# Kernel tuning notes

Hardware: AMD Instinct MI355X
Metric: run time of the kernel (lower is better)

## Reference

```python
import jax, jax.numpy as jnp
import numpy as np

B, M, D = 2048, 128, 5          # batch, max_atoms, max_degree
F_A, F_B, C = 62, 6, 128        # atom feats, bond feats, conv_width


def setup_inputs() -> dict:
    key = jax.random.key(0)
    k1, k2, k3, k4, k5 = jax.random.split(key, 5)
    atoms = jax.random.normal(k1, (B, M, F_A), dtype=jnp.float32)
    bonds = jax.random.uniform(k2, (B, M, D, F_B), dtype=jnp.float32)
    # edges in [-1, M-1]; -1 = no neighbour (padding)
    edges = jax.random.randint(k3, (B, M, D), 0, M + 1, dtype=jnp.int32) - 1
    fan = F_A + F_B
    scale = float(np.sqrt(2.0 / (fan + C)))
    W_inner = jax.random.normal(k4, (D, fan, C), dtype=jnp.float32) * scale
    b_inner = jnp.zeros((D, C), dtype=jnp.float32)
    W_self = jax.random.normal(k5, (fan, C), dtype=jnp.float32) * scale
    b_self = jnp.zeros((C,), dtype=jnp.float32)
    return {"atoms": atoms, "bonds": bonds, "edges": edges,
            "W_inner": W_inner, "b_inner": b_inner,
            "W_self": W_self, "b_self": b_self}


def reference(atoms, bonds, edges, W_inner, b_inner, W_self, b_self):
    # --- encode() of TiedGraphAutoencoder (encode_only=True) ---
    b = atoms.shape[0]
    # atom degree = number of non-(-1) entries per atom  (B, M)
    deg = jnp.sum((edges != -1).astype(jnp.float32), axis=-1)

    # neighbour_lookup: pad a zero atom at index 0, shift edges by +1,
    # batched gather -> (B, M, D, F_A)
    padded = jnp.pad(atoms, ((0, 0), (1, 0), (0, 0)))
    neigh = padded[jnp.arange(b)[:, None, None], edges + 1]

    summed_atoms = neigh.sum(axis=-2)          # (B, M, F_A)
    summed_bonds = bonds.sum(axis=-2)          # (B, M, F_B)
    summed_features = jnp.concatenate([summed_atoms, summed_bonds], axis=-1)

    # per-degree TimeDistributed Dense + relu, masked by (deg == d), summed
    h = jax.nn.relu(jnp.einsum('bmf,dfc->bmdc', summed_features, W_inner)
                    + b_inner)                 # (B, M, D, C)
    mask = (deg[..., None] == jnp.arange(D, dtype=jnp.float32)).astype(h.dtype)
    zni = jnp.einsum('bmdc,bmd->bmc', h, mask)  # (B, M, C)

    # self connection: dense on [atoms, summed_bonds]
    vxi = jnp.concatenate([atoms, summed_bonds], axis=-1)
    zxi = jax.nn.relu(vxi @ W_self + b_self)    # (B, M, C)

    return zni + zxi
```

## Files before the change

kernel.cpp:

```cpp
#include <hip/hip_runtime.h>

#define NB 2048
#define NM 128
#define ND 5
#define NFA 62
#define NFB 6
#define NFAN 68
#define NC 128
#define KTOT 96

typedef __bf16 bf16x8 __attribute__((ext_vector_type(8)));
typedef float floatx4 __attribute__((ext_vector_type(4)));

__device__ __forceinline__ unsigned short f2bf(float x) {
    unsigned u = __builtin_bit_cast(unsigned, x);
    u += 0x7FFFu + ((u >> 16) & 1u);
    return (unsigned short)(u >> 16);
}

__global__ __launch_bounds__(256) void prep_w(const float* __restrict__ W_self,
                                              unsigned short* __restrict__ wsb) {
    const int i = blockIdx.x * 256 + threadIdx.x;
    const int e     = i & 7;
    const int chunk = i >> 3;
    const int lane  = chunk & 63;
    const int cs    = chunk >> 6;
    const int ct    = cs / 3;
    const int slice = cs - 3 * ct;
    const int quad  = lane >> 4;
    const int col   = lane & 15;
    const int k     = slice * 32 + quad * 8 + e;
    const int c     = ct * 16 + col;
    unsigned short v = 0;
    if (k < NFAN) v = f2bf(W_self[k * NC + c]);
    wsb[i] = v;
}

__device__ __forceinline__ void glds16(const void* g, void* l) {
    __builtin_amdgcn_global_load_lds(
        (const __attribute__((address_space(1))) unsigned int*)g,
        (__attribute__((address_space(3))) unsigned int*)l,
        16, 0, 0);
}

__device__ __forceinline__ bf16x8 load8(const float* p) {
    float2 v0 = *(const float2*)(p);
    float2 v1 = *(const float2*)(p + 2);
    float2 v2 = *(const float2*)(p + 4);
    float2 v3 = *(const float2*)(p + 6);
    bf16x8 r;
    r[0] = (__bf16)v0.x; r[1] = (__bf16)v0.y; r[2] = (__bf16)v1.x; r[3] = (__bf16)v1.y;
    r[4] = (__bf16)v2.x; r[5] = (__bf16)v2.y; r[6] = (__bf16)v3.x; r[7] = (__bf16)v3.y;
    return r;
}

__device__ __forceinline__ bf16x8 load6bs(const float* p, const float* bs) {
    float2 v0 = *(const float2*)(p);
    float2 v1 = *(const float2*)(p + 2);
    float2 v2 = *(const float2*)(p + 4);
    float2 b01 = *(const float2*)(bs);
    bf16x8 r;
    r[0] = (__bf16)v0.x; r[1] = (__bf16)v0.y; r[2] = (__bf16)v1.x; r[3] = (__bf16)v1.y;
    r[4] = (__bf16)v2.x; r[5] = (__bf16)v2.y; r[6] = (__bf16)b01.x; r[7] = (__bf16)b01.y;
    return r;
}

__global__ __launch_bounds__(256) void tga_wave(
    const float* __restrict__ atoms,
    const float* __restrict__ bonds,
    const int*   __restrict__ edges,
    const float* __restrict__ W_inner,
    const float* __restrict__ b_inner,
    const float* __restrict__ b_self,
    const unsigned short* __restrict__ wsb,
    float* __restrict__ out)
{
    __shared__ __align__(16) unsigned short s_w[NC * KTOT];
    __shared__ __align__(16) float s_bonds[NM * ND * NFB];
    __shared__ __align__(16) float s_bsf[4][32][8];
    __shared__ float s_sf[4][64];

    const int tid  = threadIdx.x;
    const int w    = tid >> 6;
    const int lane = tid & 63;
    const int b    = blockIdx.x;
    const int m0   = w * 32;

    const float* atoms_b = atoms + (size_t)b * (NM * NFA);
    const float* bonds_b = bonds + (size_t)b * (NM * ND * NFB);
    const int*   edges_b = edges + (size_t)b * (NM * ND);
    float*       out_b   = out   + (size_t)b * (NM * NC);

    {
        const char* gw = (const char*)wsb;
        const char* gb = (const char*)bonds_b;
        char* lw = (char*)s_w;
        char* lb = (char*)s_bonds;
        for (int ch = w; ch < 24; ch += 4)
            glds16(gw + ch * 1024 + lane * 16, lw + ch * 1024);
        for (int ch = w; ch < 15; ch += 4)
            glds16(gb + ch * 1024 + lane * 16, lb + ch * 1024);
    }

    int E0 = -1, E1 = -1, E2 = -1, E3 = -1, E4 = -1, deg = ND;
    if (lane < 32) {
        const int* e = edges_b + (m0 + lane) * ND;
        E0 = e[0]; E1 = e[1]; E2 = e[2]; E3 = e[3]; E4 = e[4];
        deg = (E0 >= 0) + (E1 >= 0) + (E2 >= 0) + (E3 >= 0) + (E4 >= 0);
    }
    unsigned long long smask = __ballot((lane < 32) && (deg < ND));

    const int col = lane & 15, quad = lane >> 4;
    const int lr0 = col, lr1 = 16 + col;
    const float* p0 = atoms_b + (m0 + lr0) * NFA;
    const float* p1 = atoms_b + (m0 + lr1) * NFA;

    bf16x8 a00 = load8(p0 + quad * 8);
    bf16x8 a10 = load8(p1 + quad * 8);

    __syncthreads();

    {
        const int rb = lane >> 1, half = lane & 1;
        const float* bp = s_bonds + (m0 + rb) * (ND * NFB);
        float sb[NFB] = {0.f, 0.f, 0.f, 0.f, 0.f, 0.f};
        if (half == 0) {
            #pragma unroll
            for (int p = 0; p < 8; ++p) {
                float2 v = *(const float2*)&bp[2 * p];
                sb[(2 * p) % NFB]     += v.x;
                sb[(2 * p + 1) % NFB] += v.y;
            }
        } else {
            #pragma unroll
            for (int p = 8; p < 15; ++p) {
                float2 v = *(const float2*)&bp[2 * p];
                sb[(2 * p) % NFB]     += v.x;
                sb[(2 * p + 1) % NFB] += v.y;
            }
        }
        #pragma unroll
        for (int j = 0; j < NFB; ++j) sb[j] += __shfl_xor(sb[j], 1);
        if (half == 0) {
            *(float4*)&s_bsf[w][rb][0] = make_float4(sb[2], sb[3], sb[4], sb[5]);
            *(float2*)&s_bsf[w][rb][4] = make_float2(sb[0], sb[1]);
        }
    }
    __builtin_amdgcn_wave_barrier();

    bf16x8 a01, a11;
    if (quad < 3) {
        a01 = load8(p0 + 32 + quad * 8);
        a11 = load8(p1 + 32 + quad * 8);
    } else {
        a01 = load6bs(p0 + 56, &s_bsf[w][lr0][4]);
        a11 = load6bs(p1 + 56, &s_bsf[w][lr1][4]);
    }
    bf16x8 a02, a12;
    #pragma unroll
    for (int j = 0; j < 8; ++j) { a02[j] = (__bf16)0.f; a12[j] = (__bf16)0.f; }
    if (quad == 0) {
        float4 q0 = *(const float4*)&s_bsf[w][lr0][0];
        float4 q1 = *(const float4*)&s_bsf[w][lr1][0];
        a02[0] = (__bf16)q0.x; a02[1] = (__bf16)q0.y; a02[2] = (__bf16)q0.z; a02[3] = (__bf16)q0.w;
        a12[0] = (__bf16)q1.x; a12[1] = (__bf16)q1.y; a12[2] = (__bf16)q1.z; a12[3] = (__bf16)q1.w;
    }

    floatx4 acc[16];
    #pragma unroll
    for (int t = 0; t < 16; ++t) { floatx4 z; z[0] = z[1] = z[2] = z[3] = 0.f; acc[t] = z; }

    const unsigned short* wl = s_w + lane * 8;
    #pragma unroll
    for (int ct = 0; ct < 8; ++ct) {
        bf16x8 wf0 = *(const bf16x8*)(wl + (ct * 3 + 0) * 512);
        bf16x8 wf1 = *(const bf16x8*)(wl + (ct * 3 + 1) * 512);
        bf16x8 wf2 = *(const bf16x8*)(wl + (ct * 3 + 2) * 512);
        acc[ct]     = __builtin_amdgcn_mfma_f32_16x16x32_bf16(a00, wf0, acc[ct],     0, 0, 0);
        acc[8 + ct] = __builtin_amdgcn_mfma_f32_16x16x32_bf16(a10, wf0, acc[8 + ct], 0, 0, 0);
        acc[ct]     = __builtin_amdgcn_mfma_f32_16x16x32_bf16(a01, wf1, acc[ct],     0, 0, 0);
        acc[8 + ct] = __builtin_amdgcn_mfma_f32_16x16x32_bf16(a11, wf1, acc[8 + ct], 0, 0, 0);
        acc[ct]     = __builtin_amdgcn_mfma_f32_16x16x32_bf16(a02, wf2, acc[ct],     0, 0, 0);
        acc[8 + ct] = __builtin_amdgcn_mfma_f32_16x16x32_bf16(a12, wf2, acc[8 + ct], 0, 0, 0);
    }

    #pragma unroll
    for (int ct = 0; ct < 8; ++ct) {
        const float bias = b_self[ct * 16 + col];
        #pragma unroll
        for (int rr = 0; rr < 4; ++rr) {
            const int row0 = m0 + quad * 4 + rr;
            out_b[row0 * NC + ct * 16 + col]        = fmaxf(acc[ct][rr]     + bias, 0.f);
            out_b[(row0 + 16) * NC + ct * 16 + col] = fmaxf(acc[8 + ct][rr] + bias, 0.f);
        }
    }

    while (smask) {
        const int ml = __ffsll(smask) - 1;
        smask &= smask - 1;
        const int m  = m0 + ml;
        const int d  = __shfl(deg, ml);
        const int e0 = __shfl(E0, ml), e1 = __shfl(E1, ml), e2 = __shfl(E2, ml),
                  e3 = __shfl(E3, ml), e4 = __shfl(E4, ml);

        if (lane < NFA) {
            float sv = 0.f;
            if (e0 >= 0) sv += atoms_b[e0 * NFA + lane];
            if (e1 >= 0) sv += atoms_b[e1 * NFA + lane];
            if (e2 >= 0) sv += atoms_b[e2 * NFA + lane];
            if (e3 >= 0) sv += atoms_b[e3 * NFA + lane];
            if (e4 >= 0) sv += atoms_b[e4 * NFA + lane];
            s_sf[w][lane] = sv;
        }
        __builtin_amdgcn_wave_barrier();

        const int c0 = 2 * lane;
        float2 bi = *(const float2*)&b_inner[d * NC + c0];
        float acc0 = bi.x, acc1 = bi.y;
        const float* Wd = W_inner + (size_t)d * (NFAN * NC);
        #pragma unroll
        for (int f = 0; f < NFA; ++f) {
            const float sfv = s_sf[w][f];
            float2 wv = *(const float2*)&Wd[f * NC + c0];
            acc0 += sfv * wv.x; acc1 += sfv * wv.y;
        }
        {
            const float* bb = &s_bsf[w][ml][0];
            const float fv[6] = {bb[4], bb[5], bb[0], bb[1], bb[2], bb[3]};
            #pragma unroll
            for (int j = 0; j < NFB; ++j) {
                float2 wv = *(const float2*)&Wd[(NFA + j) * NC + c0];
                acc0 += fv[j] * wv.x; acc1 += fv[j] * wv.y;
            }
        }
        float2 cur = *(float2*)&out_b[m * NC + c0];
        cur.x += fmaxf(acc0, 0.f);
        cur.y += fmaxf(acc1, 0.f);
        *(float2*)&out_b[m * NC + c0] = cur;
        __builtin_amdgcn_wave_barrier();
    }
}

extern "C" void kernel_launch(void* const* d_in, const int* in_sizes, int n_in,
                              void* d_out, int out_size, void* d_ws, size_t ws_size,
                              hipStream_t stream) {
    const float* atoms   = (const float*)d_in[0];
    const float* bonds   = (const float*)d_in[1];
    const int*   edges   = (const int*)d_in[2];
    const float* W_inner = (const float*)d_in[3];
    const float* b_inner = (const float*)d_in[4];
    const float* W_self  = (const float*)d_in[5];
    const float* b_self  = (const float*)d_in[6];
    float* out = (float*)d_out;
    unsigned short* wsb = (unsigned short*)d_ws;

    prep_w<<<(NC * KTOT) / 256, 256, 0, stream>>>(W_self, wsb);
    tga_wave<<<NB, 256, 0, stream>>>(atoms, bonds, edges, W_inner, b_inner,
                                     b_self, wsb, out);
}
```

Before: 250.0 us.

## Process four molecules per block with double-buffered bond prefetch

Each block now handles four molecules instead of one, loading the bf16 W_self tile into LDS once per block rather than once per molecule. Bond data for the next molecule is prefetched asynchronously into a second LDS buffer while the current molecule is computed. The cost is a 4x smaller grid (512 blocks), a __syncthreads per molecule, and more LDS per block, which may reduce occupancy and parallelism on a GPU with many CUs.

```diff
diff --git a/kernel.cpp b/kernel.cpp
--- a/kernel.cpp
+++ b/kernel.cpp
@@ -8,6 +8,10 @@
 #define NFAN 68
 #define NC 128
 #define KTOT 96
+#define MPB 4
+#define NGRID (NB / MPB)
+
+#define BONDB (NM * ND * NFB * 4)
 
 typedef __bf16 bf16x8 __attribute__((ext_vector_type(8)));
 typedef float floatx4 __attribute__((ext_vector_type(4)));
@@ -65,7 +69,7 @@
     return r;
 }
 
-__global__ __launch_bounds__(256) void tga_wave(
+__global__ __launch_bounds__(256) void tga_pipe(
     const float* __restrict__ atoms,
     const float* __restrict__ bonds,
     const int*   __restrict__ edges,
@@ -76,168 +80,180 @@
     float* __restrict__ out)
 {
     __shared__ __align__(16) unsigned short s_w[NC * KTOT];
-    __shared__ __align__(16) float s_bonds[NM * ND * NFB];
+    __shared__ __align__(16) float s_bonds[2][NM * ND * NFB];
     __shared__ __align__(16) float s_bsf[4][32][8];
     __shared__ float s_sf[4][64];
 
     const int tid  = threadIdx.x;
     const int w    = tid >> 6;
     const int lane = tid & 63;
-    const int b    = blockIdx.x;
     const int m0   = w * 32;
-
-    const float* atoms_b = atoms + (size_t)b * (NM * NFA);
-    const float* bonds_b = bonds + (size_t)b * (NM * ND * NFB);
-    const int*   edges_b = edges + (size_t)b * (NM * ND);
-    float*       out_b   = out   + (size_t)b * (NM * NC);
+    const int mol0 = blockIdx.x * MPB;
+
+    const int col = lane & 15, quad = lane >> 4;
+    const int lr0 = col, lr1 = 16 + col;
 
     {
         const char* gw = (const char*)wsb;
-        const char* gb = (const char*)bonds_b;
         char* lw = (char*)s_w;
-        char* lb = (char*)s_bonds;
         for (int ch = w; ch < 24; ch += 4)
             glds16(gw + ch * 1024 + lane * 16, lw + ch * 1024);
+        const char* gb = (const char*)bonds + (size_t)mol0 * BONDB;
+        char* lb = (char*)&s_bonds[0][0];
         for (int ch = w; ch < 15; ch += 4)
             glds16(gb + ch * 1024 + lane * 16, lb + ch * 1024);
     }
-
-    int E0 = -1, E1 = -1, E2 = -1, E3 = -1, E4 = -1, deg = ND;
-    if (lane < 32) {
-        const int* e = edges_b + (m0 + lane) * ND;
-        E0 = e[0]; E1 = e[1]; E2 = e[2]; E3 = e[3]; E4 = e[4];
-        deg = (E0 >= 0) + (E1 >= 0) + (E2 >= 0) + (E3 >= 0) + (E4 >= 0);
-    }
-    unsigned long long smask = __ballot((lane < 32) && (deg < ND));
-
-    const int col = lane & 15, quad = lane >> 4;
-    const int lr0 = col, lr1 = 16 + col;
-    const float* p0 = atoms_b + (m0 + lr0) * NFA;
-    const float* p1 = atoms_b + (m0 + lr1) * NFA;
-
-    bf16x8 a00 = load8(p0 + quad * 8);
-    bf16x8 a10 = load8(p1 + quad * 8);
-
     __syncthreads();
 
-    {
-        const int rb = lane >> 1, half = lane & 1;
-        const float* bp = s_bonds + (m0 + rb) * (ND * NFB);
-        float sb[NFB] = {0.f, 0.f, 0.f, 0.f, 0.f, 0.f};
-        if (half == 0) {
+    for (int mi = 0; mi < MPB; ++mi) {
+        const int b   = mol0 + mi;
+        const int cur = mi & 1;
+
+        if (mi + 1 < MPB) {
+            const char* gb = (const char*)bonds + (size_t)(b + 1) * BONDB;
+            char* lb = (char*)&s_bonds[cur ^ 1][0];
+            for (int ch = w; ch < 15; ch += 4)
+                glds16(gb + ch * 1024 + lane * 16, lb + ch * 1024);
+        }
+
+        const float* atoms_b = atoms + (size_t)b * (NM * NFA);
+        const int*   edges_b = edges + (size_t)b * (NM * ND);
+        float*       out_b   = out   + (size_t)b * (NM * NC);
+
+        int E0 = -1, E1 = -1, E2 = -1, E3 = -1, E4 = -1, deg = ND;
+        if (lane < 32) {
+            const int* e = edges_b + (m0 + lane) * ND;
+            E0 = e[0]; E1 = e[1]; E2 = e[2]; E3 = e[3]; E4 = e[4];
+            deg = (E0 >= 0) + (E1 >= 0) + (E2 >= 0) + (E3 >= 0) + (E4 >= 0);
+        }
+        unsigned long long smask = __ballot((lane < 32) && (deg < ND));
+
+        const float* p0 = atoms_b + (m0 + lr0) * NFA;
+        const float* p1 = atoms_b + (m0 + lr1) * NFA;
+        bf16x8 a00 = load8(p0 + quad * 8);
+        bf16x8 a10 = load8(p1 + quad * 8);
+
+        {
+            const int rb = lane >> 1, half = lane & 1;
+            const float* bp = &s_bonds[cur][(m0 + rb) * (ND * NFB)];
+            float sb[NFB] = {0.f, 0.f, 0.f, 0.f, 0.f, 0.f};
+            if (half == 0) {
+                #pragma unroll
+                for (int p = 0; p < 8; ++p) {
+                    float2 v = *(const float2*)&bp[2 * p];
+                    sb[(2 * p) % NFB]     += v.x;
+                    sb[(2 * p + 1) % NFB] += v.y;
+                }
+            } else {
+                #pragma unroll
+                for (int p = 8; p < 15; ++p) {
+                    float2 v = *(const float2*)&bp[2 * p];
+                    sb[(2 * p) % NFB]     += v.x;
+                    sb[(2 * p + 1) % NFB] += v.y;
+                }
+            }
             #pragma unroll
-            for (int p = 0; p < 8; ++p) {
-                float2 v = *(const float2*)&bp[2 * p];
-                sb[(2 * p) % NFB]     += v.x;
-                sb[(2 * p + 1) % NFB] += v.y;
-            }
+            for (int j = 0; j < NFB; ++j) sb[j] += __shfl_xor(sb[j], 1);
+            if (half == 0) {
+                *(float4*)&s_bsf[w][rb][0] = make_float4(sb[2], sb[3], sb[4], sb[5]);
+                *(float2*)&s_bsf[w][rb][4] = make_float2(sb[0], sb[1]);
+            }
+        }
+        __builtin_amdgcn_wave_barrier();
+
+        bf16x8 a01, a11;
+        if (quad < 3) {
+            a01 = load8(p0 + 32 + quad * 8);
+            a11 = load8(p1 + 32 + quad * 8);
         } else {
+            a01 = load6bs(p0 + 56, &s_bsf[w][lr0][4]);
+            a11 = load6bs(p1 + 56, &s_bsf[w][lr1][4]);
+        }
+        bf16x8 a02, a12;
+        #pragma unroll
+        for (int j = 0; j < 8; ++j) { a02[j] = (__bf16)0.f; a12[j] = (__bf16)0.f; }
+        if (quad == 0) {
+            float4 q0 = *(const float4*)&s_bsf[w][lr0][0];
+            float4 q1 = *(const float4*)&s_bsf[w][lr1][0];
+            a02[0] = (__bf16)q0.x; a02[1] = (__bf16)q0.y; a02[2] = (__bf16)q0.z; a02[3] = (__bf16)q0.w;
+            a12[0] = (__bf16)q1.x; a12[1] = (__bf16)q1.y; a12[2] = (__bf16)q1.z; a12[3] = (__bf16)q1.w;
+        }
+
+        floatx4 acc[16];
+        #pragma unroll
+        for (int t = 0; t < 16; ++t) { floatx4 z; z[0] = z[1] = z[2] = z[3] = 0.f; acc[t] = z; }
+
+        const unsigned short* wl = s_w + lane * 8;
+        #pragma unroll
+        for (int ct = 0; ct < 8; ++ct) {
+            bf16x8 wf0 = *(const bf16x8*)(wl + (ct * 3 + 0) * 512);
+            bf16x8 wf1 = *(const bf16x8*)(wl + (ct * 3 + 1) * 512);
+            bf16x8 wf2 = *(const bf16x8*)(wl + (ct * 3 + 2) * 512);
+            acc[ct]     = __builtin_amdgcn_mfma_f32_16x16x32_bf16(a00, wf0, acc[ct],     0, 0, 0);
+            acc[8 + ct] = __builtin_amdgcn_mfma_f32_16x16x32_bf16(a10, wf0, acc[8 + ct], 0, 0, 0);
+            acc[ct]     = __builtin_amdgcn_mfma_f32_16x16x32_bf16(a01, wf1, acc[ct],     0, 0, 0);
+            acc[8 + ct] = __builtin_amdgcn_mfma_f32_16x16x32_bf16(a11, wf1, acc[8 + ct], 0, 0, 0);
+            acc[ct]     = __builtin_amdgcn_mfma_f32_16x16x32_bf16(a02, wf2, acc[ct],     0, 0, 0);
+            acc[8 + ct] = __builtin_amdgcn_mfma_f32_16x16x32_bf16(a12, wf2, acc[8 + ct], 0, 0, 0);
+        }
+
+        #pragma unroll
+        for (int ct = 0; ct < 8; ++ct) {
+            const float bias = b_self[ct * 16 + col];
             #pragma unroll
-            for (int p = 8; p < 15; ++p) {
-                float2 v = *(const float2*)&bp[2 * p];
-                sb[(2 * p) % NFB]     += v.x;
-                sb[(2 * p + 1) % NFB] += v.y;
-            }
-        }
-        #pragma unroll
-        for (int j = 0; j < NFB; ++j) sb[j] += __shfl_xor(sb[j], 1);
-        if (half == 0) {
-            *(float4*)&s_bsf[w][rb][0] = make_float4(sb[2], sb[3], sb[4], sb[5]);
-            *(float2*)&s_bsf[w][rb][4] = make_float2(sb[0], sb[1]);
-        }
-    }
-    __builtin_amdgcn_wave_barrier();
-
-    bf16x8 a01, a11;
-    if (quad < 3) {
-        a01 = load8(p0 + 32 + quad * 8);
-        a11 = load8(p1 + 32 + quad * 8);
-    } else {
-        a01 = load6bs(p0 + 56, &s_bsf[w][lr0][4]);
-        a11 = load6bs(p1 + 56, &s_bsf[w][lr1][4]);
-    }
-    bf16x8 a02, a12;
-    #pragma unroll
-    for (int j = 0; j < 8; ++j) { a02[j] = (__bf16)0.f; a12[j] = (__bf16)0.f; }
-    if (quad == 0) {
-        float4 q0 = *(const float4*)&s_bsf[w][lr0][0];
-        float4 q1 = *(const float4*)&s_bsf[w][lr1][0];
-        a02[0] = (__bf16)q0.x; a02[1] = (__bf16)q0.y; a02[2] = (__bf16)q0.z; a02[3] = (__bf16)q0.w;
-        a12[0] = (__bf16)q1.x; a12[1] = (__bf16)q1.y; a12[2] = (__bf16)q1.z; a12[3] = (__bf16)q1.w;
-    }
-
-    floatx4 acc[16];
-    #pragma unroll
-    for (int t = 0; t < 16; ++t) { floatx4 z; z[0] = z[1] = z[2] = z[3] = 0.f; acc[t] = z; }
-
-    const unsigned short* wl = s_w + lane * 8;
-    #pragma unroll
-    for (int ct = 0; ct < 8; ++ct) {
-        bf16x8 wf0 = *(const bf16x8*)(wl + (ct * 3 + 0) * 512);
-        bf16x8 wf1 = *(const bf16x8*)(wl + (ct * 3 + 1) * 512);
-        bf16x8 wf2 = *(const bf16x8*)(wl + (ct * 3 + 2) * 512);
-        acc[ct]     = __builtin_amdgcn_mfma_f32_16x16x32_bf16(a00, wf0, acc[ct],     0, 0, 0);
-        acc[8 + ct] = __builtin_amdgcn_mfma_f32_16x16x32_bf16(a10, wf0, acc[8 + ct], 0, 0, 0);
-        acc[ct]     = __builtin_amdgcn_mfma_f32_16x16x32_bf16(a01, wf1, acc[ct],     0, 0, 0);
-        acc[8 + ct] = __builtin_amdgcn_mfma_f32_16x16x32_bf16(a11, wf1, acc[8 + ct], 0, 0, 0);
-        acc[ct]     = __builtin_amdgcn_mfma_f32_16x16x32_bf16(a02, wf2, acc[ct],     0, 0, 0);
-        acc[8 + ct] = __builtin_amdgcn_mfma_f32_16x16x32_bf16(a12, wf2, acc[8 + ct], 0, 0, 0);
-    }
-
-    #pragma unroll
-    for (int ct = 0; ct < 8; ++ct) {
-        const float bias = b_self[ct * 16 + col];
-        #pragma unroll
-        for (int rr = 0; rr < 4; ++rr) {
-            const int row0 = m0 + quad * 4 + rr;
-            out_b[row0 * NC + ct * 16 + col]        = fmaxf(acc[ct][rr]     + bias, 0.f);
-            out_b[(row0 + 16) * NC + ct * 16 + col] = fmaxf(acc[8 + ct][rr] + bias, 0.f);
-        }
-    }
-
-    while (smask) {
-        const int ml = __ffsll(smask) - 1;
-        smask &= smask - 1;
-        const int m  = m0 + ml;
-        const int d  = __shfl(deg, ml);
-        const int e0 = __shfl(E0, ml), e1 = __shfl(E1, ml), e2 = __shfl(E2, ml),
-                  e3 = __shfl(E3, ml), e4 = __shfl(E4, ml);
-
-        if (lane < NFA) {
-            float sv = 0.f;
-            if (e0 >= 0) sv += atoms_b[e0 * NFA + lane];
-            if (e1 >= 0) sv += atoms_b[e1 * NFA + lane];
-            if (e2 >= 0) sv += atoms_b[e2 * NFA + lane];
-            if (e3 >= 0) sv += atoms_b[e3 * NFA + lane];
-            if (e4 >= 0) sv += atoms_b[e4 * NFA + lane];
-            s_sf[w][lane] = sv;
-        }
-        __builtin_amdgcn_wave_barrier();
-
-        const int c0 = 2 * lane;
-        float2 bi = *(const float2*)&b_inner[d * NC + c0];
-        float acc0 = bi.x, acc1 = bi.y;
-        const float* Wd = W_inner + (size_t)d * (NFAN * NC);
-        #pragma unroll
-        for (int f = 0; f < NFA; ++f) {
-            const float sfv = s_sf[w][f];
-            float2 wv = *(const float2*)&Wd[f * NC + c0];
-            acc0 += sfv * wv.x; acc1 += sfv * wv.y;
-        }
-        {
-            const float* bb = &s_bsf[w][ml][0];
-            const float fv[6] = {bb[4], bb[5], bb[0], bb[1], bb[2], bb[3]};
+            for (int rr = 0; rr < 4; ++rr) {
+                const int row0 = m0 + quad * 4 + rr;
+                out_b[row0 * NC + ct * 16 + col]        = fmaxf(acc[ct][rr]     + bias, 0.f);
+                out_b[(row0 + 16) * NC + ct * 16 + col] = fmaxf(acc[8 + ct][rr] + bias, 0.f);
+            }
+        }
+
+        while (smask) {
+            const int ml = __ffsll(smask) - 1;
+            smask &= smask - 1;
+            const int m  = m0 + ml;
+            const int d  = __shfl(deg, ml);
+            const int e0 = __shfl(E0, ml), e1 = __shfl(E1, ml), e2 = __shfl(E2, ml),
+                      e3 = __shfl(E3, ml), e4 = __shfl(E4, ml);
+
+            if (lane < NFA) {
+                float sv = 0.f;
+                if (e0 >= 0) sv += atoms_b[e0 * NFA + lane];
+                if (e1 >= 0) sv += atoms_b[e1 * NFA + lane];
+                if (e2 >= 0) sv += atoms_b[e2 * NFA + lane];
+                if (e3 >= 0) sv += atoms_b[e3 * NFA + lane];
+                if (e4 >= 0) sv += atoms_b[e4 * NFA + lane];
+                s_sf[w][lane] = sv;
+            }
+            __builtin_amdgcn_wave_barrier();
+
+            const int c0 = 2 * lane;
+            float2 bi = *(const float2*)&b_inner[d * NC + c0];
+            float acc0 = bi.x, acc1 = bi.y;
+            const float* Wd = W_inner + (size_t)d * (NFAN * NC);
             #pragma unroll
-            for (int j = 0; j < NFB; ++j) {
-                float2 wv = *(const float2*)&Wd[(NFA + j) * NC + c0];
-                acc0 += fv[j] * wv.x; acc1 += fv[j] * wv.y;
-            }
-        }
-        float2 cur = *(float2*)&out_b[m * NC + c0];
-        cur.x += fmaxf(acc0, 0.f);
-        cur.y += fmaxf(acc1, 0.f);
-        *(float2*)&out_b[m * NC + c0] = cur;
-        __builtin_amdgcn_wave_barrier();
+            for (int f = 0; f < NFA; ++f) {
+                const float sfv = s_sf[w][f];
+                float2 wv = *(const float2*)&Wd[f * NC + c0];
+                acc0 += sfv * wv.x; acc1 += sfv * wv.y;
+            }
+            {
+                const float* bb = &s_bsf[w][ml][0];
+                const float fv[6] = {bb[4], bb[5], bb[0], bb[1], bb[2], bb[3]};
+                #pragma unroll
+                for (int j = 0; j < NFB; ++j) {
+                    float2 wv = *(const float2*)&Wd[(NFA + j) * NC + c0];
+                    acc0 += fv[j] * wv.x; acc1 += fv[j] * wv.y;
+                }
+            }
+            float2 cur2 = *(float2*)&out_b[m * NC + c0];
+            cur2.x += fmaxf(acc0, 0.f);
+            cur2.y += fmaxf(acc1, 0.f);
+            *(float2*)&out_b[m * NC + c0] = cur2;
+            __builtin_amdgcn_wave_barrier();
+        }
+
+        __syncthreads();
     }
 }
 
@@ -255,6 +271,6 @@
     unsigned short* wsb = (unsigned short*)d_ws;
 
     prep_w<<<(NC * KTOT) / 256, 256, 0, stream>>>(W_self, wsb);
-    tga_wave<<<NB, 256, 0, stream>>>(atoms, bonds, edges, W_inner, b_inner,
-                                     b_self, wsb, out);
-}
+    tga_pipe<<<NGRID, 256, 0, stream>>>(atoms, bonds, edges, W_inner, b_inner,
+                                        b_self, wsb, out);
+}
```

After: 267.7 us. 1.07x slower.
